# Performance work log

Measured on AMD Instinct MI355X. Metric: run time of the kernel, lower is better.

## Reference

```python
import jax, jax.numpy as jnp
import numpy as np


def _binarize_ste(w):
    # forward: sign(w) in {-1, +1}; backward: identity (straight-through)
    wb = jnp.where(w >= 0, 1.0, -1.0).astype(w.dtype)
    return w + jax.lax.stop_gradient(wb - w)


def setup_inputs() -> dict:
    key = jax.random.key(0)
    k1, k2 = jax.random.split(key)
    IN, OUT, N = 2048, 2048, 8192
    x = jax.random.normal(k1, (N, IN), dtype=jnp.float32)
    # kaiming_uniform-like init: U(-bound, bound), bound = sqrt(6/in)*? (gain sqrt(5) default in torch)
    bound = float(np.sqrt(6.0 / IN))
    weight = jax.random.uniform(k2, (OUT, IN), dtype=jnp.float32, minval=-bound, maxval=bound)
    bias = jnp.zeros((OUT,), dtype=jnp.float32)
    return {"x": x, "weight": weight, "bias": bias}


def reference(x, weight, bias):
    w_binary = _binarize_ste(weight)  # [out, in], values in {-1, +1}
    # F.linear: x @ W^T + b
    return jnp.einsum('ni,oi->no', x, w_binary) + bias
```

## Files before the change

kernel.cpp:

```cpp
#include <hip/hip_runtime.h>
#include <stdint.h>


typedef __bf16 bf16x8 __attribute__((ext_vector_type(8)));
typedef float f32x16 __attribute__((ext_vector_type(16)));

typedef const __attribute__((address_space(1))) void* gas_ptr;
typedef __attribute__((address_space(3))) void* lds_ptr;

__device__ __forceinline__ unsigned short f2bf_rne(float f) {
    unsigned int u = __builtin_bit_cast(unsigned int, f);
    u += 0x7fffu + ((u >> 16) & 1u);
    return (unsigned short)(u >> 16);
}

__global__ __launch_bounds__(256) void cvt_x_kernel(const float* __restrict__ in,
                                                    unsigned short* __restrict__ out,
                                                    int n8) {
    int i = blockIdx.x * 256 + threadIdx.x;
    if (i >= n8) return;
    const float4* p = reinterpret_cast<const float4*>(in + (size_t)i * 8);
    float4 f0 = p[0], f1 = p[1];
    union { unsigned short s[8]; uint4 v; } o;
    o.s[0] = f2bf_rne(f0.x); o.s[1] = f2bf_rne(f0.y);
    o.s[2] = f2bf_rne(f0.z); o.s[3] = f2bf_rne(f0.w);
    o.s[4] = f2bf_rne(f1.x); o.s[5] = f2bf_rne(f1.y);
    o.s[6] = f2bf_rne(f1.z); o.s[7] = f2bf_rne(f1.w);
    *reinterpret_cast<uint4*>(out + (size_t)i * 8) = o.v;
}

__global__ __launch_bounds__(256) void bin_w_kernel(const float* __restrict__ in,
                                                    unsigned short* __restrict__ out,
                                                    int n4) {
    int i = blockIdx.x * 256 + threadIdx.x;
    if (i >= n4) return;
    float4 f = reinterpret_cast<const float4*>(in)[i];
    union { unsigned short s[4]; uint2 v; } o;
    o.s[0] = (f.x >= 0.f) ? 0x3F80u : 0xBF80u;
    o.s[1] = (f.y >= 0.f) ? 0x3F80u : 0xBF80u;
    o.s[2] = (f.z >= 0.f) ? 0x3F80u : 0xBF80u;
    o.s[3] = (f.w >= 0.f) ? 0x3F80u : 0xBF80u;
    reinterpret_cast<uint2*>(out)[i] = o.v;
}

#define TILE 128
#define BK   64

__global__ __launch_bounds__(256) void gemm_bin_kernel(
    const unsigned short* __restrict__ A,
    const unsigned short* __restrict__ B,
    const float* __restrict__ bias,
    float* __restrict__ C,
    int M, int N, int K)
{
    __shared__ __align__(16) unsigned char smem[32768];
    unsigned short* Als = (unsigned short*)smem;
    unsigned short* Bls = (unsigned short*)(smem + 16384);

    const int tid  = threadIdx.x;
    const int lane = tid & 63;
    const int wave = tid >> 6;
    const int wm   = wave & 1;
    const int wn   = wave >> 1;
    const int bm   = blockIdx.y;
    const int bn   = blockIdx.x;

    const unsigned short* Agb = A + (size_t)(bm * TILE) * K;
    const unsigned short* Bgb = B + (size_t)(bn * TILE) * K;

    f32x16 acc[2][2];
#pragma unroll
    for (int a = 0; a < 2; ++a)
#pragma unroll
        for (int b = 0; b < 2; ++b)
#pragma unroll
            for (int r = 0; r < 16; ++r)
                acc[a][b][r] = 0.f;

    const int lr  = lane & 31;
    const int lk  = lane >> 5;
    const int swz = lane & 7;

    int st_row[4], st_col[4];
#pragma unroll
    for (int j = 0; j < 4; ++j) {
        int g = j * 256 + tid;
        st_row[j] = g >> 3;
        st_col[j] = ((g & 7) ^ (st_row[j] & 7)) * 8;
    }

    for (int k0 = 0; k0 < K; k0 += BK) {
        __syncthreads();

#pragma unroll
        for (int j = 0; j < 4; ++j) {
            int g = j * 256 + tid;
            __builtin_amdgcn_global_load_lds(
                (gas_ptr)(Agb + (size_t)st_row[j] * K + k0 + st_col[j]),
                (lds_ptr)&Als[g * 8], 16, 0, 0);
        }
#pragma unroll
        for (int j = 0; j < 4; ++j) {
            int g = j * 256 + tid;
            __builtin_amdgcn_global_load_lds(
                (gas_ptr)(Bgb + (size_t)st_row[j] * K + k0 + st_col[j]),
                (lds_ptr)&Bls[g * 8], 16, 0, 0);
        }

        __syncthreads();

#pragma unroll
        for (int ks = 0; ks < 4; ++ks) {
            const int c = ks * 2 + lk;
            bf16x8 af[2], bfv[2];
#pragma unroll
            for (int mi = 0; mi < 2; ++mi) {
                int row = wm * 64 + mi * 32 + lr;
                af[mi] = *reinterpret_cast<const bf16x8*>(
                    &Als[(row * 8 + (c ^ swz)) * 8]);
            }
#pragma unroll
            for (int ni = 0; ni < 2; ++ni) {
                int row = wn * 64 + ni * 32 + lr;
                bfv[ni] = *reinterpret_cast<const bf16x8*>(
                    &Bls[(row * 8 + (c ^ swz)) * 8]);
            }
#pragma unroll
            for (int mi = 0; mi < 2; ++mi)
#pragma unroll
                for (int ni = 0; ni < 2; ++ni)
                    acc[mi][ni] = __builtin_amdgcn_mfma_f32_32x32x16_bf16(
                        af[mi], bfv[ni], acc[mi][ni], 0, 0, 0);
        }
    }

    float* eps = (float*)smem + wave * 2048;
    const int c4 = (lane & 15) * 4;
    const int pr = lane >> 4;
    float4 bv = *(const float4*)&bias[bn * TILE + wn * 64 + c4];

#pragma unroll
    for (int mi = 0; mi < 2; ++mi) {
        __syncthreads();
#pragma unroll
        for (int ni = 0; ni < 2; ++ni)
#pragma unroll
            for (int r = 0; r < 16; ++r) {
                int rl = (r & 3) + 8 * (r >> 2) + 4 * lk;
                eps[rl * 64 + ni * 32 + lr] = acc[mi][ni][r];
            }
        __syncthreads();
#pragma unroll
        for (int p = 0; p < 8; ++p) {
            int rl = p * 4 + pr;
            float4 v = *reinterpret_cast<const float4*>(&eps[rl * 64 + c4]);
            float4 o = {v.x + bv.x, v.y + bv.y, v.z + bv.z, v.w + bv.w};
            size_t grow = (size_t)(bm * TILE + wm * 64 + mi * 32 + rl);
            *reinterpret_cast<float4*>(&C[grow * N + bn * TILE + wn * 64 + c4]) = o;
        }
    }
}

extern "C" void kernel_launch(void* const* d_in, const int* in_sizes, int n_in,
                              void* d_out, int out_size, void* d_ws, size_t ws_size,
                              hipStream_t stream) {
    const float* x    = (const float*)d_in[0];
    const float* w    = (const float*)d_in[1];
    const float* bias = (const float*)d_in[2];
    float* out = (float*)d_out;

    const int K = 2048;
    const int N = in_sizes[2];
    const int M = in_sizes[0] / K;

    unsigned short* xb = (unsigned short*)d_ws;
    unsigned short* wb = xb + (size_t)M * K;

    const int nx8 = (M * K) / 8;
    const int nw4 = (N * K) / 4;
    cvt_x_kernel<<<(nx8 + 255) / 256, 256, 0, stream>>>(x, xb, nx8);
    bin_w_kernel<<<(nw4 + 255) / 256, 256, 0, stream>>>(w, wb, nw4);

    dim3 grid(N / TILE, M / TILE);
    gemm_bin_kernel<<<grid, 256, 0, stream>>>(xb, wb, bias, out, M, N, K);
}
```

Baseline: 199.2 us.

## Use 256x256 block tile with 4-stage async LDS pipeline and 8 waves

Rewrites the GEMM to use 512-thread blocks computing 256x256 output tiles with BK=32 and a 4-deep ring of LDS buffers filled by async global_load_lds, waiting on vmcnt so loads overlap MFMA compute. Each wave now computes a 128x64 sub-tile for more reuse per LDS read, and MFMA sections are raised in priority. The LDS-staged epilogue is replaced by direct strided stores with bias. This uses 128KB of LDS per block, which limits occupancy, and the direct epilogue stores are less coalesced.

```diff
diff --git a/kernel.cpp b/kernel.cpp
--- a/kernel.cpp
+++ b/kernel.cpp
@@ -43,122 +43,146 @@
     reinterpret_cast<uint2*>(out)[i] = o.v;
 }
 
-#define TILE 128
-#define BK   64
-
-__global__ __launch_bounds__(256) void gemm_bin_kernel(
+
+#define WAITVM(N) asm volatile("s_waitcnt vmcnt(" #N ")" ::: "memory")
+
+__device__ __forceinline__ void block_bar() {
+    asm volatile("" ::: "memory");
+    __builtin_amdgcn_s_barrier();
+    asm volatile("" ::: "memory");
+}
+
+__global__ __launch_bounds__(512, 2) void gemm_bin_kernel(
     const unsigned short* __restrict__ A,
     const unsigned short* __restrict__ B,
     const float* __restrict__ bias,
     float* __restrict__ C,
     int M, int N, int K)
 {
-    __shared__ __align__(16) unsigned char smem[32768];
-    unsigned short* Als = (unsigned short*)smem;
-    unsigned short* Bls = (unsigned short*)(smem + 16384);
+    __shared__ __align__(16) unsigned char smem_raw[131072];
+    unsigned short* const sm = (unsigned short*)smem_raw;
 
     const int tid  = threadIdx.x;
     const int lane = tid & 63;
     const int wave = tid >> 6;
-    const int wm   = wave & 1;
-    const int wn   = wave >> 1;
+    const int wm   = wave >> 2;
+    const int wn   = wave & 3;
     const int bm   = blockIdx.y;
     const int bn   = blockIdx.x;
 
-    const unsigned short* Agb = A + (size_t)(bm * TILE) * K;
-    const unsigned short* Bgb = B + (size_t)(bn * TILE) * K;
-
-    f32x16 acc[2][2];
-#pragma unroll
-    for (int a = 0; a < 2; ++a)
-#pragma unroll
-        for (int b = 0; b < 2; ++b)
-#pragma unroll
-            for (int r = 0; r < 16; ++r)
-                acc[a][b][r] = 0.f;
-
-    const int lr  = lane & 31;
-    const int lk  = lane >> 5;
-    const int swz = lane & 7;
-
-    int st_row[4], st_col[4];
-#pragma unroll
-    for (int j = 0; j < 4; ++j) {
-        int g = j * 256 + tid;
-        st_row[j] = g >> 3;
-        st_col[j] = ((g & 7) ^ (st_row[j] & 7)) * 8;
-    }
-
-    for (int k0 = 0; k0 < K; k0 += BK) {
-        __syncthreads();
-
-#pragma unroll
-        for (int j = 0; j < 4; ++j) {
-            int g = j * 256 + tid;
-            __builtin_amdgcn_global_load_lds(
-                (gas_ptr)(Agb + (size_t)st_row[j] * K + k0 + st_col[j]),
-                (lds_ptr)&Als[g * 8], 16, 0, 0);
+    const unsigned short* __restrict__ Agb = A + (size_t)(bm * 256) * K;
+    const unsigned short* __restrict__ Bgb = B + (size_t)(bn * 256) * K;
+
+    const int lr = lane & 31;
+    const int lk = lane >> 5;
+
+    int offA[4][2], offB[2][2];
+#pragma unroll
+    for (int m = 0; m < 4; ++m) {
+        const int r = wm * 128 + m * 32 + lr;
+#pragma unroll
+        for (int ks = 0; ks < 2; ++ks) {
+            const int c = ks * 2 + lk;
+            offA[m][ks] = (r * 4 + (c ^ ((r >> 1) & 3))) * 8;
         }
-#pragma unroll
-        for (int j = 0; j < 4; ++j) {
-            int g = j * 256 + tid;
-            __builtin_amdgcn_global_load_lds(
-                (gas_ptr)(Bgb + (size_t)st_row[j] * K + k0 + st_col[j]),
-                (lds_ptr)&Bls[g * 8], 16, 0, 0);
+    }
+#pragma unroll
+    for (int n = 0; n < 2; ++n) {
+        const int r = wn * 64 + n * 32 + lr;
+#pragma unroll
+        for (int ks = 0; ks < 2; ++ks) {
+            const int c = ks * 2 + lk;
+            offB[n][ks] = (r * 4 + (c ^ ((r >> 1) & 3))) * 8;
         }
-
-        __syncthreads();
-
-#pragma unroll
-        for (int ks = 0; ks < 4; ++ks) {
-            const int c = ks * 2 + lk;
-            bf16x8 af[2], bfv[2];
-#pragma unroll
-            for (int mi = 0; mi < 2; ++mi) {
-                int row = wm * 64 + mi * 32 + lr;
-                af[mi] = *reinterpret_cast<const bf16x8*>(
-                    &Als[(row * 8 + (c ^ swz)) * 8]);
+    }
+
+    int goff[2], lso[2];
+#pragma unroll
+    for (int j = 0; j < 2; ++j) {
+        const int g = j * 512 + tid;
+        const int r = g >> 2;
+        const int c = (g & 3) ^ ((r >> 1) & 3);
+        goff[j] = r * K + c * 8;
+        lso[j]  = g * 8;
+    }
+
+    f32x16 acc[4][2];
+#pragma unroll
+    for (int m = 0; m < 4; ++m)
+#pragma unroll
+        for (int n = 0; n < 2; ++n)
+#pragma unroll
+            for (int r = 0; r < 16; ++r) acc[m][n][r] = 0.f;
+
+    const int KT = K >> 5;
+
+    auto stage = [&](int ts) {
+        unsigned short* lA = sm + (ts & 3) * 16384;
+        unsigned short* lB = lA + 8192;
+        const unsigned short* ga = Agb + (size_t)ts * 32;
+        const unsigned short* gb = Bgb + (size_t)ts * 32;
+        __builtin_amdgcn_global_load_lds((gas_ptr)(ga + goff[0]), (lds_ptr)(lA + lso[0]), 16, 0, 0);
+        __builtin_amdgcn_global_load_lds((gas_ptr)(ga + goff[1]), (lds_ptr)(lA + lso[1]), 16, 0, 0);
+        __builtin_amdgcn_global_load_lds((gas_ptr)(gb + goff[0]), (lds_ptr)(lB + lso[0]), 16, 0, 0);
+        __builtin_amdgcn_global_load_lds((gas_ptr)(gb + goff[1]), (lds_ptr)(lB + lso[1]), 16, 0, 0);
+    };
+
+    auto compute = [&](int t) {
+        const unsigned short* lA = sm + (t & 3) * 16384;
+        const unsigned short* lB = lA + 8192;
+        bf16x8 af[4][2], bf[2][2];
+#pragma unroll
+        for (int m = 0; m < 4; ++m)
+#pragma unroll
+            for (int ks = 0; ks < 2; ++ks)
+                af[m][ks] = *reinterpret_cast<const bf16x8*>(lA + offA[m][ks]);
+#pragma unroll
+        for (int n = 0; n < 2; ++n)
+#pragma unroll
+            for (int ks = 0; ks < 2; ++ks)
+                bf[n][ks] = *reinterpret_cast<const bf16x8*>(lB + offB[n][ks]);
+        __builtin_amdgcn_s_setprio(1);
+#pragma unroll
+        for (int ks = 0; ks < 2; ++ks)
+#pragma unroll
+            for (int m = 0; m < 4; ++m)
+#pragma unroll
+                for (int n = 0; n < 2; ++n)
+                    acc[m][n] = __builtin_amdgcn_mfma_f32_32x32x16_bf16(
+                        af[m][ks], bf[n][ks], acc[m][n], 0, 0, 0);
+        __builtin_amdgcn_s_setprio(0);
+    };
+
+    stage(0); stage(1); stage(2);
+
+    int t = 0;
+    for (; t < KT - 3; ++t) {
+        stage(t + 3);
+        WAITVM(12);
+        block_bar();
+        compute(t);
+        block_bar();
+    }
+    WAITVM(8);  block_bar(); compute(t); block_bar(); ++t;
+    WAITVM(4);  block_bar(); compute(t); block_bar(); ++t;
+    WAITVM(0);  block_bar(); compute(t);
+
+    const int colb = bn * 256 + wn * 64;
+    const float bv0 = bias[colb + lr];
+    const float bv1 = bias[colb + 32 + lr];
+    const int r0 = bm * 256 + wm * 128 + 4 * lk;
+#pragma unroll
+    for (int m = 0; m < 4; ++m)
+#pragma unroll
+        for (int n = 0; n < 2; ++n) {
+            const float bvn = n ? bv1 : bv0;
+            float* cp = C + (size_t)(r0 + m * 32) * N + colb + n * 32 + lr;
+#pragma unroll
+            for (int r = 0; r < 16; ++r) {
+                const int rr = (r & 3) + 8 * (r >> 2);
+                cp[(size_t)rr * N] = acc[m][n][r] + bvn;
             }
-#pragma unroll
-            for (int ni = 0; ni < 2; ++ni) {
-                int row = wn * 64 + ni * 32 + lr;
-                bfv[ni] = *reinterpret_cast<const bf16x8*>(
-                    &Bls[(row * 8 + (c ^ swz)) * 8]);
-            }
-#pragma unroll
-            for (int mi = 0; mi < 2; ++mi)
-#pragma unroll
-                for (int ni = 0; ni < 2; ++ni)
-                    acc[mi][ni] = __builtin_amdgcn_mfma_f32_32x32x16_bf16(
-                        af[mi], bfv[ni], acc[mi][ni], 0, 0, 0);
         }
-    }
-
-    float* eps = (float*)smem + wave * 2048;
-    const int c4 = (lane & 15) * 4;
-    const int pr = lane >> 4;
-    float4 bv = *(const float4*)&bias[bn * TILE + wn * 64 + c4];
-
-#pragma unroll
-    for (int mi = 0; mi < 2; ++mi) {
-        __syncthreads();
-#pragma unroll
-        for (int ni = 0; ni < 2; ++ni)
-#pragma unroll
-            for (int r = 0; r < 16; ++r) {
-                int rl = (r & 3) + 8 * (r >> 2) + 4 * lk;
-                eps[rl * 64 + ni * 32 + lr] = acc[mi][ni][r];
-            }
-        __syncthreads();
-#pragma unroll
-        for (int p = 0; p < 8; ++p) {
-            int rl = p * 4 + pr;
-            float4 v = *reinterpret_cast<const float4*>(&eps[rl * 64 + c4]);
-            float4 o = {v.x + bv.x, v.y + bv.y, v.z + bv.z, v.w + bv.w};
-            size_t grow = (size_t)(bm * TILE + wm * 64 + mi * 32 + rl);
-            *reinterpret_cast<float4*>(&C[grow * N + bn * TILE + wn * 64 + c4]) = o;
-        }
-    }
 }
 
 extern "C" void kernel_launch(void* const* d_in, const int* in_sizes, int n_in,
@@ -181,6 +205,6 @@
     cvt_x_kernel<<<(nx8 + 255) / 256, 256, 0, stream>>>(x, xb, nx8);
     bin_w_kernel<<<(nw4 + 255) / 256, 256, 0, stream>>>(w, wb, nw4);
 
-    dim3 grid(N / TILE, M / TILE);
-    gemm_bin_kernel<<<grid, 256, 0, stream>>>(xb, wb, bias, out, M, N, K);
-}
+    dim3 grid(N / 256, M / 256);
+    gemm_bin_kernel<<<grid, 512, 0, stream>>>(xb, wb, bias, out, M, N, K);
+}
```

Result: no change. 201.3 us (+1.0%).
